# Performance work log

Hardware: AMD Instinct MI355X
Metric: run time of the kernel (lower is better)

The kernel has to match this reference:

```python
import jax, jax.numpy as jnp
import numpy as np

B, N, C, H = 2, 2048, 768, 12
D = C // H  # head dim = 64


def _rotate_half(x):
    d2 = x.shape[-1] // 2
    x1, x2 = x[..., :d2], x[..., d2:]
    return jnp.concatenate([-x2, x1], axis=-1)


def _apply_rope(x, sin, cos):
    # x: [B,H,N,D], sin/cos: [N,D] -> broadcast over (B,H)
    return x * cos[None, None] + _rotate_half(x) * sin[None, None]


def setup_inputs() -> dict:
    key = jax.random.key(0)
    ks = jax.random.split(key, 7)
    x = jax.random.normal(ks[0], (B, N, C), dtype=jnp.float32)
    sin_spatial = jax.random.normal(ks[1], (N, D), dtype=jnp.float32)
    cos_spatial = jax.random.normal(ks[2], (N, D), dtype=jnp.float32)
    s = 1.0 / np.sqrt(C)
    W_qkv = jax.random.uniform(ks[3], (C, 3 * C), jnp.float32, -s, s)
    b_qkv = jax.random.uniform(ks[4], (3 * C,), jnp.float32, -s, s)
    W_out = jax.random.uniform(ks[5], (C, C), jnp.float32, -s, s)
    b_out = jax.random.uniform(ks[6], (C,), jnp.float32, -s, s)
    return {"x": x, "sin_spatial": sin_spatial, "cos_spatial": cos_spatial,
            "W_qkv": W_qkv, "b_qkv": b_qkv, "W_out": W_out, "b_out": b_out}


def reference(x, sin_spatial, cos_spatial, W_qkv, b_qkv, W_out, b_out):
    qkv = x @ W_qkv + b_qkv                       # [B,N,3C]
    qkv = qkv.reshape(B, N, 3, H, D).transpose(2, 0, 3, 1, 4)  # [3,B,H,N,D]
    q, k, v = qkv[0], qkv[1], qkv[2]
    q = _apply_rope(q, sin_spatial, cos_spatial)
    k = _apply_rope(k, sin_spatial, cos_spatial)
    att = jnp.einsum('bhqd,bhkd->bhqk', q, k) * (D ** -0.5)
    att = jax.nn.softmax(att, axis=-1)            # dropout is identity (eval)
    y = jnp.einsum('bhqk,bhkd->bhqd', att, v)     # [B,H,N,D]
    y = y.transpose(0, 2, 1, 3).reshape(B, N, C)
    return y @ W_out + b_out
```

## Files before the change

kernel.cpp:

```cpp
#include <hip/hip_runtime.h>
#include <hip/hip_bf16.h>

#define BB 2
#define NN 2048
#define CC 768
#define HH 12
#define DD 64
#define MM 4096
#define N3 2304

typedef __attribute__((ext_vector_type(8))) short bf16x8;
typedef __attribute__((ext_vector_type(4))) float f32x4;

#define QSCALE 0.18033688011112043f

__device__ __forceinline__ unsigned short f2bf(float f) {
    union { float f; unsigned u; } v; v.f = f;
    unsigned r = v.u + 0x7FFFu + ((v.u >> 16) & 1u);
    return (unsigned short)(r >> 16);
}

__device__ __forceinline__ short f2bf_rn(float f) {
    union { __hip_bfloat16 h; short s; } v;
    v.h = __float2bfloat16(f);
    return v.s;
}

__device__ __forceinline__ float exp2_hw(float x) {
    float r;
    asm("v_exp_f32 %0, %1" : "=v"(r) : "v"(x));
    return r;
}

__device__ __forceinline__ bf16x8 ld_frag(const unsigned short* p) {
    bf16x8 r;
    __builtin_memcpy(&r, p, 8);
    __builtin_memcpy((char*)&r + 8, p + 16, 8);
    return r;
}

__global__ void k_cvt(const float* __restrict__ s, unsigned short* __restrict__ d, int n4) {
    int i = blockIdx.x * blockDim.x + threadIdx.x;
    int st = gridDim.x * blockDim.x;
    for (; i < n4; i += st) {
        float4 v = ((const float4*)s)[i];
        ushort4 o;
        o.x = f2bf(v.x); o.y = f2bf(v.y); o.z = f2bf(v.z); o.w = f2bf(v.w);
        ((ushort4*)d)[i] = o;
    }
}

__global__ void k_cvtT(const float* __restrict__ s, unsigned short* __restrict__ d,
                       int R, int Cc) {
    __shared__ unsigned short t[64][72];
    const int c0 = blockIdx.x * 64, r0 = blockIdx.y * 64;
    const int tr = threadIdx.x >> 4;
    const int tc = (threadIdx.x & 15) * 4;
#pragma unroll
    for (int i = 0; i < 4; i++) {
        int r = tr + i * 16;
        float4 v = *(const float4*)(s + (size_t)(r0 + r) * Cc + c0 + tc);
        t[tc + 0][r] = f2bf(v.x);
        t[tc + 1][r] = f2bf(v.y);
        t[tc + 2][r] = f2bf(v.z);
        t[tc + 3][r] = f2bf(v.w);
    }
    __syncthreads();
    const int wr = threadIdx.x >> 2;
    const int wc = (threadIdx.x & 3) * 16;
    *(uint4*)(d + (size_t)(c0 + wr) * R + r0 + wc)     = *(uint4*)&t[wr][wc];
    *(uint4*)(d + (size_t)(c0 + wr) * R + r0 + wc + 8) = *(uint4*)&t[wr][wc + 8];
}

__launch_bounds__(256)
__global__ void k_qkv(const unsigned short* __restrict__ xb,
                      const unsigned short* __restrict__ wt,
                      const float* __restrict__ bias,
                      const float* __restrict__ sinp,
                      const float* __restrict__ cosp,
                      unsigned short* __restrict__ qws,
                      unsigned short* __restrict__ kws,
                      unsigned short* __restrict__ vws) {
    __shared__ unsigned short As[128][40];
    __shared__ unsigned short Bs[64][40];
    const int tid = threadIdx.x;
    const int lane = tid & 63, w = tid >> 6;
    const int ql = lane & 15, lg = lane >> 4;
    const int row0 = blockIdx.x * 128;
    const int j0 = blockIdx.y * 64;

    f32x4 acc[2][4];
#pragma unroll
    for (int a = 0; a < 2; a++)
#pragma unroll
        for (int b = 0; b < 4; b++) acc[a][b] = f32x4{0.f, 0.f, 0.f, 0.f};

    const int ar = tid >> 1, ac = (tid & 1) * 16;
    const int jr = tid >> 2, kc = (tid & 3) * 8;

    for (int k0 = 0; k0 < CC; k0 += 32) {
        uint4 av0 = *(const uint4*)(xb + (size_t)(row0 + ar) * CC + k0 + ac);
        uint4 av1 = *(const uint4*)(xb + (size_t)(row0 + ar) * CC + k0 + ac + 8);
        uint4 bv  = *(const uint4*)(wt + (size_t)(j0 + jr) * CC + k0 + kc);
        *(uint4*)&As[ar][ac]     = av0;
        *(uint4*)&As[ar][ac + 8] = av1;
        *(uint4*)&Bs[jr][kc]     = bv;
        __syncthreads();

        bf16x8 af[2], bfr[4];
#pragma unroll
        for (int fr = 0; fr < 2; fr++) af[fr] = ld_frag(&As[w * 32 + fr * 16 + ql][lg * 4]);
#pragma unroll
        for (int fn = 0; fn < 4; fn++) bfr[fn] = ld_frag(&Bs[fn * 16 + ql][lg * 4]);
#pragma unroll
        for (int fr = 0; fr < 2; fr++)
#pragma unroll
            for (int fn = 0; fn < 4; fn++)
                acc[fr][fn] = __builtin_amdgcn_mfma_f32_16x16x32_bf16(af[fr], bfr[fn], acc[fr][fn], 0, 0, 0);
        __syncthreads();
    }

    float vals[2][4][4];
#pragma unroll
    for (int fr = 0; fr < 2; fr++)
#pragma unroll
        for (int fn = 0; fn < 4; fn++) {
            float bj = bias[j0 + fn * 16 + ql];
#pragma unroll
            for (int r = 0; r < 4; r++) vals[fr][fn][r] = acc[fr][fn][r] + bj;
        }
    const int t = j0 / CC;
    const int h = (j0 % CC) >> 6;
    if (t < 2) {
        unsigned short* outp = (t == 0) ? qws : kws;
        const float qs = (t == 0) ? QSCALE : 1.0f;
#pragma unroll
        for (int fr = 0; fr < 2; fr++)
#pragma unroll
            for (int r = 0; r < 4; r++) {
                int m = row0 + w * 32 + fr * 16 + lg * 4 + r;
                int b = m >> 11, n = m & (NN - 1);
#pragma unroll
                for (int fn = 0; fn < 4; fn++) {
                    int d = fn * 16 + ql;
                    float cv = cosp[n * DD + d], sv = sinp[n * DD + d];
                    float other = vals[fr][fn ^ 2][r];
                    float rv = (vals[fr][fn][r] * cv + ((fn < 2) ? -other : other) * sv) * qs;
                    outp[((size_t)(b * HH + h) * NN + n) * DD + d] = f2bf(rv);
                }
            }
    } else {
#pragma unroll
        for (int fr = 0; fr < 2; fr++)
#pragma unroll
            for (int r = 0; r < 4; r++) {
                int m = row0 + w * 32 + fr * 16 + lg * 4 + r;
                int b = m >> 11, n = m & (NN - 1);
#pragma unroll
                for (int fn = 0; fn < 4; fn++) {
                    int d = fn * 16 + ql;
                    vws[((size_t)(b * HH + h) * DD + d) * NN + n] = f2bf(vals[fr][fn][r]);
                }
            }
    }
}

__launch_bounds__(256)
__global__ void k_attn(const unsigned short* __restrict__ qws,
                       const unsigned short* __restrict__ kws,
                       const unsigned short* __restrict__ vws,
                       unsigned short* __restrict__ yws) {
    __shared__ unsigned short Ks[2][64][72];
    __shared__ unsigned short Vs[2][64][72];
    const int tid = threadIdx.x;
    const int lane = tid & 63, w = tid >> 6;
    const int ql = lane & 15, lg = lane >> 4;
    const int d0 = blockIdx.x;
    const int bh = (d0 & 7) + 8 * (d0 >> 8);
    const int qb = (d0 >> 3) & 31;
    const int qw = qb * 64 + w * 16;
    const unsigned short* Qp = qws + (size_t)bh * NN * DD;
    const unsigned short* Kp = kws + (size_t)bh * NN * DD;
    const unsigned short* Vp = vws + (size_t)bh * DD * NN;

    bf16x8 qf[2];
#pragma unroll
    for (int kb = 0; kb < 2; kb++)
        qf[kb] = ld_frag(Qp + (size_t)(qw + ql) * DD + kb * 32 + lg * 4);

    f32x4 oacc[4];
#pragma unroll
    for (int a = 0; a < 4; a++) oacc[a] = f32x4{0.f, 0.f, 0.f, 0.f};
    float mrun = -1e30f, lrun = 0.f;

    const int sr = tid >> 2, sc = (tid & 3) * 16;

    *(uint4*)&Ks[0][sr][sc]     = *(const uint4*)(Kp + (size_t)sr * DD + sc);
    *(uint4*)&Ks[0][sr][sc + 8] = *(const uint4*)(Kp + (size_t)sr * DD + sc + 8);
    *(uint4*)&Vs[0][sr][sc]     = *(const uint4*)(Vp + (size_t)sr * NN + sc);
    *(uint4*)&Vs[0][sr][sc + 8] = *(const uint4*)(Vp + (size_t)sr * NN + sc + 8);
    __syncthreads();

    const int NT = NN / 64;
    int cur = 0;
    for (int kt = 0; kt < NT; kt++) {
        uint4 kn0, kn1, vn0, vn1;
        const bool hasn = (kt + 1 < NT);
        if (hasn) {
            kn0 = *(const uint4*)(Kp + (size_t)((kt + 1) * 64 + sr) * DD + sc);
            kn1 = *(const uint4*)(Kp + (size_t)((kt + 1) * 64 + sr) * DD + sc + 8);
            vn0 = *(const uint4*)(Vp + (size_t)sr * NN + (kt + 1) * 64 + sc);
            vn1 = *(const uint4*)(Vp + (size_t)sr * NN + (kt + 1) * 64 + sc + 8);
        }
        const unsigned short (*Kc)[72] = Ks[cur];
        const unsigned short (*Vc)[72] = Vs[cur];

        f32x4 sacc[4];
#pragma unroll
        for (int a = 0; a < 4; a++) sacc[a] = f32x4{0.f, 0.f, 0.f, 0.f};
        __builtin_amdgcn_s_setprio(1);
#pragma unroll
        for (int kb = 0; kb < 2; kb++) {
            bf16x8 kf[4];
#pragma unroll
            for (int fr = 0; fr < 4; fr++) kf[fr] = ld_frag(&Kc[fr * 16 + ql][kb * 32 + lg * 4]);
#pragma unroll
            for (int fr = 0; fr < 4; fr++)
                sacc[fr] = __builtin_amdgcn_mfma_f32_16x16x32_bf16(kf[fr], qf[kb], sacc[fr], 0, 0, 0);
        }
        __builtin_amdgcn_s_setprio(0);

        float m0 = fmaxf(fmaxf(sacc[0][0], sacc[0][1]), fmaxf(sacc[0][2], sacc[0][3]));
        float m1 = fmaxf(fmaxf(sacc[1][0], sacc[1][1]), fmaxf(sacc[1][2], sacc[1][3]));
        float m2 = fmaxf(fmaxf(sacc[2][0], sacc[2][1]), fmaxf(sacc[2][2], sacc[2][3]));
        float m3 = fmaxf(fmaxf(sacc[3][0], sacc[3][1]), fmaxf(sacc[3][2], sacc[3][3]));
        float tm = fmaxf(fmaxf(m0, m1), fmaxf(m2, m3));
        tm = fmaxf(tm, __shfl_xor(tm, 16));
        tm = fmaxf(tm, __shfl_xor(tm, 32));
        if (__any(tm > mrun + 8.0f)) {
            float mn = fmaxf(mrun, tm);
            float scl = exp2_hw(mrun - mn);
            lrun *= scl;
#pragma unroll
            for (int db = 0; db < 4; db++) oacc[db] *= scl;
            mrun = mn;
        }
        float ts = 0.f;
#pragma unroll
        for (int fr = 0; fr < 4; fr++)
#pragma unroll
            for (int r = 0; r < 4; r++) {
                float p = exp2_hw(sacc[fr][r] - mrun);
                sacc[fr][r] = p;
                ts += p;
            }
        ts += __shfl_xor(ts, 16);
        ts += __shfl_xor(ts, 32);
        lrun += ts;

        bf16x8 pB[2];
#pragma unroll
        for (int kkb = 0; kkb < 2; kkb++) {
            bf16x8 t8;
#pragma unroll
            for (int e = 0; e < 8; e++)
                t8[e] = f2bf_rn(sacc[kkb * 2 + (e >> 2)][e & 3]);
            pB[kkb] = t8;
        }

        __builtin_amdgcn_s_setprio(1);
#pragma unroll
        for (int db = 0; db < 4; db++) {
            bf16x8 va[2];
#pragma unroll
            for (int kkb = 0; kkb < 2; kkb++) va[kkb] = ld_frag(&Vc[db * 16 + ql][kkb * 32 + lg * 4]);
#pragma unroll
            for (int kkb = 0; kkb < 2; kkb++)
                oacc[db] = __builtin_amdgcn_mfma_f32_16x16x32_bf16(va[kkb], pB[kkb], oacc[db], 0, 0, 0);
        }
        __builtin_amdgcn_s_setprio(0);

        if (hasn) {
            *(uint4*)&Ks[cur ^ 1][sr][sc]     = kn0;
            *(uint4*)&Ks[cur ^ 1][sr][sc + 8] = kn1;
            *(uint4*)&Vs[cur ^ 1][sr][sc]     = vn0;
            *(uint4*)&Vs[cur ^ 1][sr][sc + 8] = vn1;
            __syncthreads();
            cur ^= 1;
        }
    }

    const int b = bh / HH, h = bh % HH;
    float inv = 1.0f / lrun;
    int q = qw + ql;
    unsigned short* yp = yws + (size_t)(b * NN + q) * CC + h * DD + lg * 4;
#pragma unroll
    for (int db = 0; db < 4; db++) {
        ushort4 o;
        o.x = f2bf(oacc[db][0] * inv);
        o.y = f2bf(oacc[db][1] * inv);
        o.z = f2bf(oacc[db][2] * inv);
        o.w = f2bf(oacc[db][3] * inv);
        *(ushort4*)(yp + db * 16) = o;
    }
}

__launch_bounds__(256)
__global__ void k_out(const unsigned short* __restrict__ yb,
                      const unsigned short* __restrict__ wt,
                      const float* __restrict__ bias,
                      float* __restrict__ out) {
    __shared__ unsigned short As[128][40];
    __shared__ unsigned short Bs[64][40];
    const int tid = threadIdx.x;
    const int lane = tid & 63, w = tid >> 6;
    const int ql = lane & 15, lg = lane >> 4;
    const int row0 = blockIdx.x * 128;
    const int j0 = blockIdx.y * 64;

    f32x4 acc[2][4];
#pragma unroll
    for (int a = 0; a < 2; a++)
#pragma unroll
        for (int b = 0; b < 4; b++) acc[a][b] = f32x4{0.f, 0.f, 0.f, 0.f};

    const int ar = tid >> 1, ac = (tid & 1) * 16;
    const int jr = tid >> 2, kc = (tid & 3) * 8;

    for (int k0 = 0; k0 < CC; k0 += 32) {
        uint4 av0 = *(const uint4*)(yb + (size_t)(row0 + ar) * CC + k0 + ac);
        uint4 av1 = *(const uint4*)(yb + (size_t)(row0 + ar) * CC + k0 + ac + 8);
        uint4 bv  = *(const uint4*)(wt + (size_t)(j0 + jr) * CC + k0 + kc);
        *(uint4*)&As[ar][ac]     = av0;
        *(uint4*)&As[ar][ac + 8] = av1;
        *(uint4*)&Bs[jr][kc]     = bv;
        __syncthreads();

        bf16x8 af[2], bfr[4];
#pragma unroll
        for (int fr = 0; fr < 2; fr++) af[fr] = ld_frag(&As[w * 32 + fr * 16 + ql][lg * 4]);
#pragma unroll
        for (int fn = 0; fn < 4; fn++) bfr[fn] = ld_frag(&Bs[fn * 16 + ql][lg * 4]);
#pragma unroll
        for (int fr = 0; fr < 2; fr++)
#pragma unroll
            for (int fn = 0; fn < 4; fn++)
                acc[fr][fn] = __builtin_amdgcn_mfma_f32_16x16x32_bf16(af[fr], bfr[fn], acc[fr][fn], 0, 0, 0);
        __syncthreads();
    }

#pragma unroll
    for (int fr = 0; fr < 2; fr++)
#pragma unroll
        for (int fn = 0; fn < 4; fn++) {
            float bj = bias[j0 + fn * 16 + ql];
#pragma unroll
            for (int r = 0; r < 4; r++) {
                int m = row0 + w * 32 + fr * 16 + lg * 4 + r;
                out[(size_t)m * CC + j0 + fn * 16 + ql] = acc[fr][fn][r] + bj;
            }
        }
}

extern "C" void kernel_launch(void* const* d_in, const int* in_sizes, int n_in,
                              void* d_out, int out_size, void* d_ws, size_t ws_size,
                              hipStream_t stream) {
    const float* x    = (const float*)d_in[0];
    const float* sinp = (const float*)d_in[1];
    const float* cosp = (const float*)d_in[2];
    const float* wqkv = (const float*)d_in[3];
    const float* bqkv = (const float*)d_in[4];
    const float* wout = (const float*)d_in[5];
    const float* bout = (const float*)d_in[6];
    float* out = (float*)d_out;
    char* ws = (char*)d_ws;

    unsigned short* xb  = (unsigned short*)(ws);
    unsigned short* wqb = (unsigned short*)(ws + 6291456);
    unsigned short* wob = (unsigned short*)(ws + 9830400);
    unsigned short* qws = (unsigned short*)(ws + 11010048);
    unsigned short* kws = (unsigned short*)(ws + 17301504);
    unsigned short* vws = (unsigned short*)(ws + 23592960);
    unsigned short* yws = (unsigned short*)(ws + 29884416);
    if (ws_size < 36175872) return;

    k_cvt<<<dim3(512), dim3(256), 0, stream>>>(x, xb, MM * CC / 4);
    k_cvtT<<<dim3(36, 12), dim3(256), 0, stream>>>(wqkv, wqb, CC, N3);
    k_cvtT<<<dim3(12, 12), dim3(256), 0, stream>>>(wout, wob, CC, CC);
    k_qkv<<<dim3(32, 36), dim3(256), 0, stream>>>(xb, wqb, bqkv, sinp, cosp, qws, kws, vws);
    k_attn<<<dim3(768), dim3(256), 0, stream>>>(qws, kws, vws, yws);
    k_out<<<dim3(32, 12), dim3(256), 0, stream>>>(yws, wob, bout, out);
}
```

Measured before the change: 140.1 us.

## Give each attention wave 32 queries and permute K/V layout for 16-byte fragment loads

The attention kernel now runs 2 waves per block, each handling 32 query rows (two 16-row MFMA tiles). Each K and V fragment loaded from LDS is reused for two MFMAs, halving LDS reads per MFMA. The QKV epilogue stores K columns and V sequence positions in a permuted order so a fragment becomes one contiguous 16-byte LDS read instead of two 8-byte reads. The cost is more registers per wave (doubled accumulators and score tiles) and fewer waves per block to hide latency, which may lower occupancy.

Result: faster. 136.3 us (-2.7%).

```diff
diff --git a/kernel.cpp b/kernel.cpp
--- a/kernel.cpp
+++ b/kernel.cpp
@@ -14,6 +14,7 @@
 
 #define QSCALE 0.18033688011112043f
 
+
 __device__ __forceinline__ unsigned short f2bf(float f) {
     union { float f; unsigned u; } v; v.f = f;
     unsigned r = v.u + 0x7FFFu + ((v.u >> 16) & 1u);
@@ -36,6 +37,12 @@
     bf16x8 r;
     __builtin_memcpy(&r, p, 8);
     __builtin_memcpy((char*)&r + 8, p + 16, 8);
+    return r;
+}
+
+__device__ __forceinline__ bf16x8 ld_frag16(const unsigned short* p) {
+    bf16x8 r;
+    __builtin_memcpy(&r, p, 16);
     return r;
 }
 
@@ -146,7 +153,9 @@
                     float cv = cosp[n * DD + d], sv = sinp[n * DD + d];
                     float other = vals[fr][fn ^ 2][r];
                     float rv = (vals[fr][fn][r] * cv + ((fn < 2) ? -other : other) * sv) * qs;
-                    outp[((size_t)(b * HH + h) * NN + n) * DD + d] = f2bf(rv);
+                    int dcol = (t == 0) ? d
+                             : ((fn >> 1) * 32 + (ql >> 2) * 8 + (fn & 1) * 4 + (ql & 3));
+                    outp[((size_t)(b * HH + h) * NN + n) * DD + dcol] = f2bf(rv);
                 }
             }
     } else {
@@ -156,16 +165,17 @@
             for (int r = 0; r < 4; r++) {
                 int m = row0 + w * 32 + fr * 16 + lg * 4 + r;
                 int b = m >> 11, n = m & (NN - 1);
+                int ncol = (n & ~31) + lg * 8 + (fr & 1) * 4 + r;
 #pragma unroll
                 for (int fn = 0; fn < 4; fn++) {
                     int d = fn * 16 + ql;
-                    vws[((size_t)(b * HH + h) * DD + d) * NN + n] = f2bf(vals[fr][fn][r]);
+                    vws[((size_t)(b * HH + h) * DD + d) * NN + ncol] = f2bf(vals[fr][fn][r]);
                 }
             }
     }
 }
 
-__launch_bounds__(256)
+__launch_bounds__(128)
 __global__ void k_attn(const unsigned short* __restrict__ qws,
                        const unsigned short* __restrict__ kws,
                        const unsigned short* __restrict__ vws,
@@ -178,94 +188,109 @@
     const int d0 = blockIdx.x;
     const int bh = (d0 & 7) + 8 * (d0 >> 8);
     const int qb = (d0 >> 3) & 31;
-    const int qw = qb * 64 + w * 16;
+    const int qw = qb * 64 + w * 32;
     const unsigned short* Qp = qws + (size_t)bh * NN * DD;
     const unsigned short* Kp = kws + (size_t)bh * NN * DD;
     const unsigned short* Vp = vws + (size_t)bh * DD * NN;
 
-    bf16x8 qf[2];
-#pragma unroll
-    for (int kb = 0; kb < 2; kb++)
-        qf[kb] = ld_frag(Qp + (size_t)(qw + ql) * DD + kb * 32 + lg * 4);
-
-    f32x4 oacc[4];
-#pragma unroll
-    for (int a = 0; a < 4; a++) oacc[a] = f32x4{0.f, 0.f, 0.f, 0.f};
-    float mrun = -1e30f, lrun = 0.f;
-
-    const int sr = tid >> 2, sc = (tid & 3) * 16;
-
-    *(uint4*)&Ks[0][sr][sc]     = *(const uint4*)(Kp + (size_t)sr * DD + sc);
-    *(uint4*)&Ks[0][sr][sc + 8] = *(const uint4*)(Kp + (size_t)sr * DD + sc + 8);
-    *(uint4*)&Vs[0][sr][sc]     = *(const uint4*)(Vp + (size_t)sr * NN + sc);
-    *(uint4*)&Vs[0][sr][sc + 8] = *(const uint4*)(Vp + (size_t)sr * NN + sc + 8);
+    bf16x8 qf[2][2];
+#pragma unroll
+    for (int fn = 0; fn < 2; fn++)
+#pragma unroll
+        for (int kb = 0; kb < 2; kb++)
+            qf[fn][kb] = ld_frag(Qp + (size_t)(qw + fn * 16 + ql) * DD + kb * 32 + lg * 4);
+
+    f32x4 oacc[4][2];
+#pragma unroll
+    for (int a = 0; a < 4; a++)
+#pragma unroll
+        for (int b = 0; b < 2; b++) oacc[a][b] = f32x4{0.f, 0.f, 0.f, 0.f};
+    float mrun[2] = {-1e30f, -1e30f}, lrun[2] = {0.f, 0.f};
+
+    const int srow = tid >> 1;
+    const int shalf = (tid & 1) * 32;
+
+#pragma unroll
+    for (int j = 0; j < 4; j++) {
+        *(uint4*)&Ks[0][srow][shalf + j * 8] = *(const uint4*)(Kp + (size_t)srow * DD + shalf + j * 8);
+        *(uint4*)&Vs[0][srow][shalf + j * 8] = *(const uint4*)(Vp + (size_t)srow * NN + shalf + j * 8);
+    }
     __syncthreads();
 
     const int NT = NN / 64;
     int cur = 0;
     for (int kt = 0; kt < NT; kt++) {
-        uint4 kn0, kn1, vn0, vn1;
+        uint4 kn[4], vn[4];
         const bool hasn = (kt + 1 < NT);
         if (hasn) {
-            kn0 = *(const uint4*)(Kp + (size_t)((kt + 1) * 64 + sr) * DD + sc);
-            kn1 = *(const uint4*)(Kp + (size_t)((kt + 1) * 64 + sr) * DD + sc + 8);
-            vn0 = *(const uint4*)(Vp + (size_t)sr * NN + (kt + 1) * 64 + sc);
-            vn1 = *(const uint4*)(Vp + (size_t)sr * NN + (kt + 1) * 64 + sc + 8);
+#pragma unroll
+            for (int j = 0; j < 4; j++) {
+                kn[j] = *(const uint4*)(Kp + (size_t)((kt + 1) * 64 + srow) * DD + shalf + j * 8);
+                vn[j] = *(const uint4*)(Vp + (size_t)srow * NN + (kt + 1) * 64 + shalf + j * 8);
+            }
         }
         const unsigned short (*Kc)[72] = Ks[cur];
         const unsigned short (*Vc)[72] = Vs[cur];
 
-        f32x4 sacc[4];
-#pragma unroll
-        for (int a = 0; a < 4; a++) sacc[a] = f32x4{0.f, 0.f, 0.f, 0.f};
+        f32x4 sacc[4][2];
+#pragma unroll
+        for (int a = 0; a < 4; a++)
+#pragma unroll
+            for (int b = 0; b < 2; b++) sacc[a][b] = f32x4{0.f, 0.f, 0.f, 0.f};
         __builtin_amdgcn_s_setprio(1);
 #pragma unroll
         for (int kb = 0; kb < 2; kb++) {
             bf16x8 kf[4];
 #pragma unroll
-            for (int fr = 0; fr < 4; fr++) kf[fr] = ld_frag(&Kc[fr * 16 + ql][kb * 32 + lg * 4]);
-#pragma unroll
             for (int fr = 0; fr < 4; fr++)
-                sacc[fr] = __builtin_amdgcn_mfma_f32_16x16x32_bf16(kf[fr], qf[kb], sacc[fr], 0, 0, 0);
+                kf[fr] = ld_frag16(&Kc[fr * 16 + ql][kb * 32 + lg * 8]);
+#pragma unroll
+            for (int fr = 0; fr < 4; fr++)
+#pragma unroll
+                for (int fn = 0; fn < 2; fn++)
+                    sacc[fr][fn] = __builtin_amdgcn_mfma_f32_16x16x32_bf16(kf[fr], qf[fn][kb], sacc[fr][fn], 0, 0, 0);
         }
         __builtin_amdgcn_s_setprio(0);
 
-        float m0 = fmaxf(fmaxf(sacc[0][0], sacc[0][1]), fmaxf(sacc[0][2], sacc[0][3]));
-        float m1 = fmaxf(fmaxf(sacc[1][0], sacc[1][1]), fmaxf(sacc[1][2], sacc[1][3]));
-        float m2 = fmaxf(fmaxf(sacc[2][0], sacc[2][1]), fmaxf(sacc[2][2], sacc[2][3]));
-        float m3 = fmaxf(fmaxf(sacc[3][0], sacc[3][1]), fmaxf(sacc[3][2], sacc[3][3]));
-        float tm = fmaxf(fmaxf(m0, m1), fmaxf(m2, m3));
-        tm = fmaxf(tm, __shfl_xor(tm, 16));
-        tm = fmaxf(tm, __shfl_xor(tm, 32));
-        if (__any(tm > mrun + 8.0f)) {
-            float mn = fmaxf(mrun, tm);
-            float scl = exp2_hw(mrun - mn);
-            lrun *= scl;
-#pragma unroll
-            for (int db = 0; db < 4; db++) oacc[db] *= scl;
-            mrun = mn;
-        }
-        float ts = 0.f;
-#pragma unroll
-        for (int fr = 0; fr < 4; fr++)
-#pragma unroll
-            for (int r = 0; r < 4; r++) {
-                float p = exp2_hw(sacc[fr][r] - mrun);
-                sacc[fr][r] = p;
-                ts += p;
-            }
-        ts += __shfl_xor(ts, 16);
-        ts += __shfl_xor(ts, 32);
-        lrun += ts;
-
-        bf16x8 pB[2];
-#pragma unroll
-        for (int kkb = 0; kkb < 2; kkb++) {
-            bf16x8 t8;
-#pragma unroll
-            for (int e = 0; e < 8; e++)
-                t8[e] = f2bf_rn(sacc[kkb * 2 + (e >> 2)][e & 3]);
-            pB[kkb] = t8;
+        bf16x8 pB[2][2];
+#pragma unroll
+        for (int fn = 0; fn < 2; fn++) {
+            float ma = fmaxf(fmaxf(sacc[0][fn][0], sacc[0][fn][1]), fmaxf(sacc[0][fn][2], sacc[0][fn][3]));
+            float mb = fmaxf(fmaxf(sacc[1][fn][0], sacc[1][fn][1]), fmaxf(sacc[1][fn][2], sacc[1][fn][3]));
+            float mc = fmaxf(fmaxf(sacc[2][fn][0], sacc[2][fn][1]), fmaxf(sacc[2][fn][2], sacc[2][fn][3]));
+            float md = fmaxf(fmaxf(sacc[3][fn][0], sacc[3][fn][1]), fmaxf(sacc[3][fn][2], sacc[3][fn][3]));
+            float tm = fmaxf(fmaxf(ma, mb), fmaxf(mc, md));
+            tm = fmaxf(tm, __shfl_xor(tm, 16));
+            tm = fmaxf(tm, __shfl_xor(tm, 32));
+            if (__any(tm > mrun[fn] + 8.0f)) {
+                float mn = fmaxf(mrun[fn], tm);
+                float scl = exp2_hw(mrun[fn] - mn);
+                lrun[fn] *= scl;
+#pragma unroll
+                for (int db = 0; db < 4; db++) oacc[db][fn] *= scl;
+                mrun[fn] = mn;
+            }
+            float ts = 0.f;
+#pragma unroll
+            for (int fr = 0; fr < 4; fr++)
+#pragma unroll
+                for (int r = 0; r < 4; r++) {
+                    float p = exp2_hw(sacc[fr][fn][r] - mrun[fn]);
+                    sacc[fr][fn][r] = p;
+                    ts += p;
+                }
+            ts += __shfl_xor(ts, 16);
+            ts += __shfl_xor(ts, 32);
+            lrun[fn] += ts;
+
+#pragma unroll
+            for (int kkb = 0; kkb < 2; kkb++) {
+                bf16x8 t8;
+#pragma unroll
+                for (int e = 0; e < 8; e++)
+                    t8[e] = f2bf_rn(sacc[kkb * 2 + (e >> 2)][fn][e & 3]);
+                pB[fn][kkb] = t8;
+            }
         }
 
         __builtin_amdgcn_s_setprio(1);
@@ -273,35 +298,42 @@
         for (int db = 0; db < 4; db++) {
             bf16x8 va[2];
 #pragma unroll
-            for (int kkb = 0; kkb < 2; kkb++) va[kkb] = ld_frag(&Vc[db * 16 + ql][kkb * 32 + lg * 4]);
-#pragma unroll
             for (int kkb = 0; kkb < 2; kkb++)
-                oacc[db] = __builtin_amdgcn_mfma_f32_16x16x32_bf16(va[kkb], pB[kkb], oacc[db], 0, 0, 0);
+                va[kkb] = ld_frag16(&Vc[db * 16 + ql][kkb * 32 + lg * 8]);
+#pragma unroll
+            for (int kkb = 0; kkb < 2; kkb++)
+#pragma unroll
+                for (int fn = 0; fn < 2; fn++)
+                    oacc[db][fn] = __builtin_amdgcn_mfma_f32_16x16x32_bf16(va[kkb], pB[fn][kkb], oacc[db][fn], 0, 0, 0);
         }
         __builtin_amdgcn_s_setprio(0);
 
         if (hasn) {
-            *(uint4*)&Ks[cur ^ 1][sr][sc]     = kn0;
-            *(uint4*)&Ks[cur ^ 1][sr][sc + 8] = kn1;
-            *(uint4*)&Vs[cur ^ 1][sr][sc]     = vn0;
-            *(uint4*)&Vs[cur ^ 1][sr][sc + 8] = vn1;
+#pragma unroll
+            for (int j = 0; j < 4; j++) {
+                *(uint4*)&Ks[cur ^ 1][srow][shalf + j * 8] = kn[j];
+                *(uint4*)&Vs[cur ^ 1][srow][shalf + j * 8] = vn[j];
+            }
             __syncthreads();
             cur ^= 1;
         }
     }
 
     const int b = bh / HH, h = bh % HH;
-    float inv = 1.0f / lrun;
-    int q = qw + ql;
-    unsigned short* yp = yws + (size_t)(b * NN + q) * CC + h * DD + lg * 4;
-#pragma unroll
-    for (int db = 0; db < 4; db++) {
-        ushort4 o;
-        o.x = f2bf(oacc[db][0] * inv);
-        o.y = f2bf(oacc[db][1] * inv);
-        o.z = f2bf(oacc[db][2] * inv);
-        o.w = f2bf(oacc[db][3] * inv);
-        *(ushort4*)(yp + db * 16) = o;
+#pragma unroll
+    for (int fn = 0; fn < 2; fn++) {
+        float inv = 1.0f / lrun[fn];
+        int q = qw + fn * 16 + ql;
+        unsigned short* yp = yws + (size_t)(b * NN + q) * CC + h * DD + lg * 4;
+#pragma unroll
+        for (int db = 0; db < 4; db++) {
+            ushort4 o;
+            o.x = f2bf(oacc[db][fn][0] * inv);
+            o.y = f2bf(oacc[db][fn][1] * inv);
+            o.z = f2bf(oacc[db][fn][2] * inv);
+            o.w = f2bf(oacc[db][fn][3] * inv);
+            *(ushort4*)(yp + db * 16) = o;
+        }
     }
 }
 
@@ -388,6 +420,6 @@
     k_cvtT<<<dim3(36, 12), dim3(256), 0, stream>>>(wqkv, wqb, CC, N3);
     k_cvtT<<<dim3(12, 12), dim3(256), 0, stream>>>(wout, wob, CC, CC);
     k_qkv<<<dim3(32, 36), dim3(256), 0, stream>>>(xb, wqb, bqkv, sinp, cosp, qws, kws, vws);
-    k_attn<<<dim3(768), dim3(256), 0, stream>>>(qws, kws, vws, yws);
+    k_attn<<<dim3(768), dim3(128), 0, stream>>>(qws, kws, vws, yws);
     k_out<<<dim3(32, 12), dim3(256), 0, stream>>>(yws, wob, bout, out);
 }
```
